# Kernel optimization log

Hardware: AMD Instinct MI355X
Metric: run time of the kernel (lower is better)

The kernel has to match this reference:

```python
import jax, jax.numpy as jnp
import numpy as np

MASK_THRED = 1        # init kwarg mask_thred
TRIPLE_WEIGHT = 1.0   # init kwarg triple_weight (scales gradient of shifted branch)
NEG = -1e30
EPS = 1e-8


def setup_inputs() -> dict:
    key = jax.random.key(0)
    k1, k2 = jax.random.split(key)
    x = jax.random.normal(k1, (2, 128, 96, 96), dtype=jnp.float32)
    mask = jax.random.randint(k2, (96, 96), 0, 2, dtype=jnp.int32)
    return {"x": x, "mask": mask}


def reference(x, mask):
    # x: (B, C, H, W); former = x[:, :C//2], latter = x[:, C//2:]
    B, C, H, W = x.shape
    c2 = C // 2
    hw = H * W

    # shift_sz=1, stride=1, mask_thred=1 -> a location is 'masked' iff mask >= 1
    flag = mask.reshape(hw) >= MASK_THRED  # (hw,) True = inside hole

    former, latter = x[:, :c2], x[:, c2:]

    # similarity path is non-differentiable in the original (hard argmax, detached latter)
    lat = jax.lax.stop_gradient(latter).reshape(B, c2, hw).transpose(0, 2, 1)  # (B, hw, c2)
    # original normalizes only the candidate (non-masked) patches (NCC filters)
    lat_n = lat / jnp.maximum(jnp.linalg.norm(lat, axis=-1, keepdims=True), EPS)

    # cross-correlation of every location against every (normalized) candidate
    sim = jnp.einsum('bic,bjc->bij', lat, lat_n)  # (B, hw, hw)
    # only non-masked locations are valid candidates j
    sim = jnp.where(flag[None, None, :], NEG, sim)
    idx = jnp.argmax(sim, axis=-1)  # (B, hw) nearest non-masked neighbor per location

    # shift: copy the FORMER feature from the matched non-masked location
    fmr = former.reshape(B, c2, hw).transpose(0, 2, 1)  # (B, hw, c2)
    gathered = jnp.take_along_axis(fmr, idx[:, :, None], axis=1)  # (B, hw, c2)

    # triple_weight scales only the gradient of the shifted branch (fwd unchanged)
    tw = jnp.float32(TRIPLE_WEIGHT)
    gathered = gathered * tw + jax.lax.stop_gradient(gathered * (1.0 - tw))

    # shifted features only at masked locations, zero elsewhere
    shift = jnp.where(flag[None, :, None], gathered, jnp.float32(0.0))
    shift = shift.transpose(0, 2, 1).reshape(B, c2, H, W)

    # triple: (former, latter, shifted) -> (B, 3*C//2, H, W)
    return jnp.concatenate([former, latter, shift], axis=1)
```

## Files before the change

### kernel.cpp

```cpp
#include <hip/hip_runtime.h>
#include <math.h>

#define HW 9216
#define C2 64
#define NSTRIP 288
#define NCH 16
#define EPSN 1e-8f

typedef _Float16 f16x8  __attribute__((ext_vector_type(8)));
typedef float    f32x16 __attribute__((ext_vector_type(16)));

__global__ void prep_kernel(const float* __restrict__ x, const int* __restrict__ mask,
                            int* __restrict__ ilist, int* __restrict__ jlist,
                            int* __restrict__ slotmap, int* __restrict__ counts,
                            float* __restrict__ invAll, unsigned long long* __restrict__ amax) {
    if (blockIdx.x < 576) {
        int t = blockIdx.x * 256 + threadIdx.x;
        int cc = t & 7;
        int pb = t >> 3;
        int b = pb / HW, p = pb - b * HW;
        const float* xl = x + (size_t)(b * 128 + 64) * HW + p;
        float ss = 0.f;
#pragma unroll
        for (int e = 0; e < 8; e++) { float w = xl[(size_t)(cc * 8 + e) * HW]; ss = fmaf(w, w, ss); }
        ss += __shfl_xor(ss, 1, 64);
        ss += __shfl_xor(ss, 2, 64);
        ss += __shfl_xor(ss, 4, 64);
        if (cc == 0) {
            invAll[pb] = 1.0f / fmaxf(sqrtf(ss), EPSN);
            amax[pb] = 0ull;
        }
    } else {
        int t = threadIdx.x;
        int base = t * 36;
        unsigned long long fl = 0ull; int cnt = 0;
#pragma unroll
        for (int k = 0; k < 36; k++) {
            int f = (mask[base + k] >= 1) ? 1 : 0;
            fl |= (unsigned long long)f << k;
            cnt += f;
        }
        int lane = t & 63, wave = t >> 6;
        int v = cnt;
#pragma unroll
        for (int off = 1; off < 64; off <<= 1) {
            int u = __shfl_up(v, off, 64);
            if (lane >= off) v += u;
        }
        __shared__ int wsum[4];
        if (lane == 63) wsum[wave] = v;
        __syncthreads();
        int woff = 0;
#pragma unroll
        for (int w = 0; w < 4; w++) if (w < wave) woff += wsum[w];
        int incl = v + woff;
        int excl = incl - cnt;
        int posF = excl, posU = base - excl;
#pragma unroll
        for (int k = 0; k < 36; k++) {
            int p = base + k;
            if ((fl >> k) & 1ull) { slotmap[p] = posF | 0x80000000; ilist[posF++] = p; }
            else                  { slotmap[p] = posU;              jlist[posU++] = p; }
        }
        if (t == 255) { counts[0] = incl; counts[1] = HW - incl; }
    }
}

__global__ void pack_kernel(const float* __restrict__ x, const int* __restrict__ slotmap,
                            const float* __restrict__ invAll,
                            _Float16* __restrict__ aH, _Float16* __restrict__ aL,
                            _Float16* __restrict__ bH, _Float16* __restrict__ bL) {
    int p = blockIdx.x * 256 + threadIdx.x;
    int cc = blockIdx.y;
    int b = blockIdx.z;
    int sm = slotmap[p];
    int flagged = (sm >> 31) & 1;
    int slot = sm & 0x7fffffff;
    const float* xl = x + (size_t)(b * 128 + 64) * HW + p;
    float scale = flagged ? 1.0f : invAll[b * HW + p];
    f16x8 hh, ll;
#pragma unroll
    for (int e = 0; e < 8; e++) {
        float w = xl[(size_t)(cc * 8 + e) * HW] * scale;
        _Float16 h = (_Float16)w;
        hh[e] = h;
        ll[e] = (_Float16)((w - (float)h) * 2048.0f);
    }
    int ks = cc >> 1, g = cc & 1;
    int strip = slot >> 5, ln = slot & 31;
    size_t off = ((((size_t)b * NSTRIP + strip) * 4 + ks) * 64 + (g * 32 + ln)) * 8;
    _Float16* dh = flagged ? aH : bH;
    _Float16* dl = flagged ? aL : bL;
    *(f16x8*)(dh + off) = hh;
    *(f16x8*)(dl + off) = ll;
}

__device__ __forceinline__ unsigned int ordf(float f) {
    unsigned int u = __float_as_uint(f);
    return (u & 0x80000000u) ? ~u : (u | 0x80000000u);
}

__global__ __launch_bounds__(256, 2) void argmax_kernel(
    const _Float16* __restrict__ aH, const _Float16* __restrict__ aL,
    const _Float16* __restrict__ bH, const _Float16* __restrict__ bL,
    const int* __restrict__ ilist, const int* __restrict__ counts,
    unsigned long long* __restrict__ amax)
{
    int ni = counts[0];
    if (blockIdx.x * 256 >= ni) return;
    int nj = counts[1];
    int njt = (nj + 31) >> 5;
    int tpc = (njt + NCH - 1) / NCH;
    int s = blockIdx.y;
    int jt0 = s * tpc, jt1 = min(jt0 + tpc, njt);
    if (jt0 >= jt1) return;
    int b = blockIdx.z;
    int wave = threadIdx.x >> 6, l = threadIdx.x & 63;
    int base = (blockIdx.x * 4 + wave) * 64;
    int g = l >> 5, ln = l & 31;
    int strip0 = base >> 5;

    __shared__ f16x8 lds[2][8][64];

    const f16x8* apH = (const f16x8*)aH + ((size_t)b * NSTRIP + strip0) * 256 + l;
    const f16x8* apL = (const f16x8*)aL + ((size_t)b * NSTRIP + strip0) * 256 + l;
    f16x8 xh0 = apH[0],   xh1 = apH[64],  xh2 = apH[128], xh3 = apH[192];
    f16x8 xl0 = apL[0],   xl1 = apL[64],  xl2 = apL[128], xl3 = apL[192];
    f16x8 yh0 = apH[256], yh1 = apH[320], yh2 = apH[384], yh3 = apH[448];
    f16x8 yl0 = apL[256], yl1 = apL[320], yl2 = apL[384], yl3 = apL[448];

    int f0 = wave * 2;
    const f16x8* s0 = (const f16x8*)((f0 < 4) ? bH : bL) +
                      (size_t)b * NSTRIP * 256 + (size_t)(f0 & 3) * 64 + l;
    const f16x8* s1 = (const f16x8*)((f0 + 1 < 4) ? bH : bL) +
                      (size_t)b * NSTRIP * 256 + (size_t)((f0 + 1) & 3) * 64 + l;

    {
        f16x8 t0 = s0[(size_t)jt0 * 256];
        f16x8 t1 = s1[(size_t)jt0 * 256];
        lds[0][f0][l] = t0;
        lds[0][f0 + 1][l] = t1;
    }
    __syncthreads();

    float bv0 = -INFINITY, bv1 = -INFINITY;
    int bj0 = -1, bj1 = -1;
    int cur = 0;

    for (int jt = jt0; jt < jt1; ++jt, cur ^= 1) {
        f16x8 n0, n1;
        bool more = (jt + 1 < jt1);
        if (more) {
            n0 = s0[(size_t)(jt + 1) * 256];
            n1 = s1[(size_t)(jt + 1) * 256];
        }
        f16x8 bh0 = lds[cur][0][l], bh1 = lds[cur][1][l];
        f16x8 bh2 = lds[cur][2][l], bh3 = lds[cur][3][l];
        f16x8 bl0 = lds[cur][4][l], bl1 = lds[cur][5][l];
        f16x8 bl2 = lds[cur][6][l], bl3 = lds[cur][7][l];
        f32x16 cH0 = {}, cC0 = {}, cH1 = {}, cC1 = {};
        cH0 = __builtin_amdgcn_mfma_f32_32x32x16_f16(bh0, xh0, cH0, 0, 0, 0);
        cC0 = __builtin_amdgcn_mfma_f32_32x32x16_f16(bh0, xl0, cC0, 0, 0, 0);
        cC0 = __builtin_amdgcn_mfma_f32_32x32x16_f16(bl0, xh0, cC0, 0, 0, 0);
        cH0 = __builtin_amdgcn_mfma_f32_32x32x16_f16(bh1, xh1, cH0, 0, 0, 0);
        cC0 = __builtin_amdgcn_mfma_f32_32x32x16_f16(bh1, xl1, cC0, 0, 0, 0);
        cC0 = __builtin_amdgcn_mfma_f32_32x32x16_f16(bl1, xh1, cC0, 0, 0, 0);
        cH0 = __builtin_amdgcn_mfma_f32_32x32x16_f16(bh2, xh2, cH0, 0, 0, 0);
        cC0 = __builtin_amdgcn_mfma_f32_32x32x16_f16(bh2, xl2, cC0, 0, 0, 0);
        cC0 = __builtin_amdgcn_mfma_f32_32x32x16_f16(bl2, xh2, cC0, 0, 0, 0);
        cH0 = __builtin_amdgcn_mfma_f32_32x32x16_f16(bh3, xh3, cH0, 0, 0, 0);
        cC0 = __builtin_amdgcn_mfma_f32_32x32x16_f16(bh3, xl3, cC0, 0, 0, 0);
        cC0 = __builtin_amdgcn_mfma_f32_32x32x16_f16(bl3, xh3, cC0, 0, 0, 0);
        cH1 = __builtin_amdgcn_mfma_f32_32x32x16_f16(bh0, yh0, cH1, 0, 0, 0);
        cC1 = __builtin_amdgcn_mfma_f32_32x32x16_f16(bh0, yl0, cC1, 0, 0, 0);
        cC1 = __builtin_amdgcn_mfma_f32_32x32x16_f16(bl0, yh0, cC1, 0, 0, 0);
        cH1 = __builtin_amdgcn_mfma_f32_32x32x16_f16(bh1, yh1, cH1, 0, 0, 0);
        cC1 = __builtin_amdgcn_mfma_f32_32x32x16_f16(bh1, yl1, cC1, 0, 0, 0);
        cC1 = __builtin_amdgcn_mfma_f32_32x32x16_f16(bl1, yh1, cC1, 0, 0, 0);
        cH1 = __builtin_amdgcn_mfma_f32_32x32x16_f16(bh2, yh2, cH1, 0, 0, 0);
        cC1 = __builtin_amdgcn_mfma_f32_32x32x16_f16(bh2, yl2, cC1, 0, 0, 0);
        cC1 = __builtin_amdgcn_mfma_f32_32x32x16_f16(bl2, yh2, cC1, 0, 0, 0);
        cH1 = __builtin_amdgcn_mfma_f32_32x32x16_f16(bh3, yh3, cH1, 0, 0, 0);
        cC1 = __builtin_amdgcn_mfma_f32_32x32x16_f16(bh3, yl3, cC1, 0, 0, 0);
        cC1 = __builtin_amdgcn_mfma_f32_32x32x16_f16(bl3, yh3, cC1, 0, 0, 0);
        int jb = jt << 5;
#pragma unroll
        for (int r = 0; r < 16; ++r) {
            int row = (r & 3) + 8 * (r >> 2) + 4 * g;
            int j = jb + row;
            float v0 = fmaf(cC0[r], 4.8828125e-4f , cH0[r]);
            float v1 = fmaf(cC1[r], 4.8828125e-4f, cH1[r]);
            if (j < nj && v0 > bv0) { bv0 = v0; bj0 = j; }
            if (j < nj && v1 > bv1) { bv1 = v1; bj1 = j; }
        }
        if (more) {
            lds[cur ^ 1][f0][l] = n0;
            lds[cur ^ 1][f0 + 1][l] = n1;
        }
        __syncthreads();
    }

    unsigned long long k0 = ((unsigned long long)ordf(bv0) << 32) |
                            (unsigned long long)(~(unsigned int)bj0);
    unsigned long long k1 = ((unsigned long long)ordf(bv1) << 32) |
                            (unsigned long long)(~(unsigned int)bj1);
    unsigned long long o0 = __shfl_xor(k0, 32, 64);
    unsigned long long o1 = __shfl_xor(k1, 32, 64);
    if (o0 > k0) k0 = o0;
    if (o1 > k1) k1 = o1;
    int il0 = base + ln, il1 = base + 32 + ln;
    if (g == 0) {
        if (il0 < ni && (unsigned)(k0 >> 32) > 0x007FFFFFu)
            atomicMax(&amax[(size_t)b * HW + ilist[il0]], k0);
        if (il1 < ni && (unsigned)(k1 >> 32) > 0x007FFFFFu)
            atomicMax(&amax[(size_t)b * HW + ilist[il1]], k1);
    }
}

__global__ void epilogue_kernel(const float4* __restrict__ x4, const float* __restrict__ x,
                                const int* __restrict__ mask,
                                const unsigned long long* __restrict__ amax,
                                const int* __restrict__ jlist, float4* __restrict__ out4) {
    const int q = HW / 4;
    int t = blockIdx.x * blockDim.x + threadIdx.x;
    if (t >= 2 * 192 * q) return;
    int pos4 = t % q;
    int c = (t / q) % 192;
    int b = t / (192 * q);
    if (c < 128) {
        out4[t] = x4[((size_t)b * 128 + c) * q + pos4];
    } else {
        float4 v = make_float4(0.f, 0.f, 0.f, 0.f);
        float* vp = &v.x;
        int pos = pos4 * 4;
        const float* xf = x + (size_t)(b * 128 + (c - 128)) * HW;
#pragma unroll
        for (int k = 0; k < 4; k++) {
            int p = pos + k;
            if (mask[p] >= 1) {
                unsigned long long key = amax[(size_t)b * HW + p];
                int j = 0;
                if (key != 0ull) j = jlist[(int)(~(unsigned int)key)];
                vp[k] = xf[j];
            }
        }
        out4[t] = v;
    }
}

extern "C" void kernel_launch(void* const* d_in, const int* in_sizes, int n_in,
                              void* d_out, int out_size, void* d_ws, size_t ws_size,
                              hipStream_t stream) {
    const float* x = (const float*)d_in[0];
    const int* mask = (const int*)d_in[1];
    float4* out4 = (float4*)d_out;

    char* ws = (char*)d_ws;
    int*   counts  = (int*)ws;
    int*   ilist   = (int*)(ws + 128);
    int*   jlist   = (int*)(ws + 36992);
    int*   slotmap = (int*)(ws + 73856);
    unsigned long long* amax = (unsigned long long*)(ws + 110720);
    float* invAll  = (float*)(ws + 258176);
    _Float16* aH = (_Float16*)(ws + 331904);
    _Float16* aL = (_Float16*)(ws + 331904 + 1 * 2359296);
    _Float16* bH = (_Float16*)(ws + 331904 + 2 * 2359296);
    _Float16* bL = (_Float16*)(ws + 331904 + 3 * 2359296);

    prep_kernel<<<577, 256, 0, stream>>>(x, mask, ilist, jlist, slotmap, counts,
                                         invAll, amax);
    {
        dim3 grid(HW / 256, 8, 2);
        pack_kernel<<<grid, 256, 0, stream>>>(x, slotmap, invAll, aH, aL, bH, bL);
    }
    {
        dim3 grid(NSTRIP / 8, NCH, 2);
        argmax_kernel<<<grid, 256, 0, stream>>>(aH, aL, bH, bL, ilist, counts, amax);
    }
    {
        int n = 2 * 192 * (HW / 4);
        epilogue_kernel<<<(n + 255) / 256, 256, 0, stream>>>((const float4*)x, x, mask,
                                                             amax, jlist, out4);
    }
}
```

Measured before the change: 109.7 us.

## Drop mask compaction; compute full dense similarity with bitmask filtering

```diff
diff --git a/kernel.cpp b/kernel.cpp
--- a/kernel.cpp
+++ b/kernel.cpp
@@ -2,7 +2,6 @@
 #include <math.h>
 
 #define HW 9216
-#define C2 64
 #define NSTRIP 288
 #define NCH 16
 #define EPSN 1e-8f
@@ -11,88 +10,52 @@
 typedef float    f32x16 __attribute__((ext_vector_type(16)));
 
 __global__ void prep_kernel(const float* __restrict__ x, const int* __restrict__ mask,
-                            int* __restrict__ ilist, int* __restrict__ jlist,
-                            int* __restrict__ slotmap, int* __restrict__ counts,
-                            float* __restrict__ invAll, unsigned long long* __restrict__ amax) {
-    if (blockIdx.x < 576) {
-        int t = blockIdx.x * 256 + threadIdx.x;
-        int cc = t & 7;
-        int pb = t >> 3;
-        int b = pb / HW, p = pb - b * HW;
-        const float* xl = x + (size_t)(b * 128 + 64) * HW + p;
-        float ss = 0.f;
-#pragma unroll
-        for (int e = 0; e < 8; e++) { float w = xl[(size_t)(cc * 8 + e) * HW]; ss = fmaf(w, w, ss); }
-        ss += __shfl_xor(ss, 1, 64);
-        ss += __shfl_xor(ss, 2, 64);
-        ss += __shfl_xor(ss, 4, 64);
-        if (cc == 0) {
-            invAll[pb] = 1.0f / fmaxf(sqrtf(ss), EPSN);
-            amax[pb] = 0ull;
-        }
-    } else {
-        int t = threadIdx.x;
-        int base = t * 36;
-        unsigned long long fl = 0ull; int cnt = 0;
-#pragma unroll
-        for (int k = 0; k < 36; k++) {
-            int f = (mask[base + k] >= 1) ? 1 : 0;
-            fl |= (unsigned long long)f << k;
-            cnt += f;
-        }
-        int lane = t & 63, wave = t >> 6;
-        int v = cnt;
-#pragma unroll
-        for (int off = 1; off < 64; off <<= 1) {
-            int u = __shfl_up(v, off, 64);
-            if (lane >= off) v += u;
-        }
-        __shared__ int wsum[4];
-        if (lane == 63) wsum[wave] = v;
-        __syncthreads();
-        int woff = 0;
-#pragma unroll
-        for (int w = 0; w < 4; w++) if (w < wave) woff += wsum[w];
-        int incl = v + woff;
-        int excl = incl - cnt;
-        int posF = excl, posU = base - excl;
-#pragma unroll
-        for (int k = 0; k < 36; k++) {
-            int p = base + k;
-            if ((fl >> k) & 1ull) { slotmap[p] = posF | 0x80000000; ilist[posF++] = p; }
-            else                  { slotmap[p] = posU;              jlist[posU++] = p; }
-        }
-        if (t == 255) { counts[0] = incl; counts[1] = HW - incl; }
-    }
-}
-
-__global__ void pack_kernel(const float* __restrict__ x, const int* __restrict__ slotmap,
-                            const float* __restrict__ invAll,
+                            unsigned* __restrict__ fw, unsigned long long* __restrict__ amax,
                             _Float16* __restrict__ aH, _Float16* __restrict__ aL,
                             _Float16* __restrict__ bH, _Float16* __restrict__ bL) {
-    int p = blockIdx.x * 256 + threadIdx.x;
-    int cc = blockIdx.y;
-    int b = blockIdx.z;
-    int sm = slotmap[p];
-    int flagged = (sm >> 31) & 1;
-    int slot = sm & 0x7fffffff;
+    if (blockIdx.x == 288) {
+        for (int w = threadIdx.x; w < NSTRIP; w += 256) {
+            const int* mp = mask + w * 32;
+            unsigned m = 0;
+#pragma unroll
+            for (int k = 0; k < 32; k++) m |= (mp[k] >= 1 ? 1u : 0u) << k;
+            fw[w] = m;
+        }
+        return;
+    }
+    int t = blockIdx.x * 256 + threadIdx.x;
+    int sub = t & 63;
+    int q = sub >> 4;
+    int pb = ((t >> 6) << 4) | (sub & 15);
+    int b = pb / HW, p = pb - b * HW;
     const float* xl = x + (size_t)(b * 128 + 64) * HW + p;
-    float scale = flagged ? 1.0f : invAll[b * HW + p];
-    f16x8 hh, ll;
-#pragma unroll
-    for (int e = 0; e < 8; e++) {
-        float w = xl[(size_t)(cc * 8 + e) * HW] * scale;
-        _Float16 h = (_Float16)w;
-        hh[e] = h;
-        ll[e] = (_Float16)((w - (float)h) * 2048.0f);
-    }
-    int ks = cc >> 1, g = cc & 1;
-    int strip = slot >> 5, ln = slot & 31;
-    size_t off = ((((size_t)b * NSTRIP + strip) * 4 + ks) * 64 + (g * 32 + ln)) * 8;
-    _Float16* dh = flagged ? aH : bH;
-    _Float16* dl = flagged ? aL : bL;
-    *(f16x8*)(dh + off) = hh;
-    *(f16x8*)(dl + off) = ll;
+    float v[16]; float ss = 0.f;
+#pragma unroll
+    for (int e = 0; e < 16; e++) { float w0 = xl[(size_t)(q * 16 + e) * HW]; v[e] = w0; ss = fmaf(w0, w0, ss); }
+    ss += __shfl_xor(ss, 16, 64);
+    ss += __shfl_xor(ss, 32, 64);
+    float inv = 1.0f / fmaxf(sqrtf(ss), EPSN);
+    if (q == 0) amax[pb] = 0ull;
+    int tile = p >> 5, lnp = p & 31;
+#pragma unroll
+    for (int h = 0; h < 2; h++) {
+        size_t off = ((((size_t)b * NSTRIP + tile) * 4 + q) * 64 + h * 32 + lnp) * 8;
+        f16x8 hh, ll;
+#pragma unroll
+        for (int e = 0; e < 8; e++) {
+            float w0 = v[h * 8 + e];
+            _Float16 hv = (_Float16)w0;
+            hh[e] = hv; ll[e] = (_Float16)((w0 - (float)hv) * 2048.0f);
+        }
+        *(f16x8*)(aH + off) = hh; *(f16x8*)(aL + off) = ll;
+#pragma unroll
+        for (int e = 0; e < 8; e++) {
+            float w0 = v[h * 8 + e] * inv;
+            _Float16 hv = (_Float16)w0;
+            hh[e] = hv; ll[e] = (_Float16)((w0 - (float)hv) * 2048.0f);
+        }
+        *(f16x8*)(bH + off) = hh; *(f16x8*)(bL + off) = ll;
+    }
 }
 
 __device__ __forceinline__ unsigned int ordf(float f) {
@@ -103,18 +66,11 @@
 __global__ __launch_bounds__(256, 2) void argmax_kernel(
     const _Float16* __restrict__ aH, const _Float16* __restrict__ aL,
     const _Float16* __restrict__ bH, const _Float16* __restrict__ bL,
-    const int* __restrict__ ilist, const int* __restrict__ counts,
-    unsigned long long* __restrict__ amax)
+    const unsigned* __restrict__ fw, unsigned long long* __restrict__ amax)
 {
-    int ni = counts[0];
-    if (blockIdx.x * 256 >= ni) return;
-    int nj = counts[1];
-    int njt = (nj + 31) >> 5;
-    int tpc = (njt + NCH - 1) / NCH;
-    int s = blockIdx.y;
-    int jt0 = s * tpc, jt1 = min(jt0 + tpc, njt);
-    if (jt0 >= jt1) return;
-    int b = blockIdx.z;
+    const int tpc = NSTRIP / NCH;
+    int b = blockIdx.z, s = blockIdx.y;
+    int jt0 = s * tpc, jt1 = jt0 + tpc;
     int wave = threadIdx.x >> 6, l = threadIdx.x & 63;
     int base = (blockIdx.x * 4 + wave) * 64;
     int g = l >> 5, ln = l & 31;
@@ -184,14 +140,18 @@
         cC1 = __builtin_amdgcn_mfma_f32_32x32x16_f16(bh3, yl3, cC1, 0, 0, 0);
         cC1 = __builtin_amdgcn_mfma_f32_32x32x16_f16(bl3, yh3, cC1, 0, 0, 0);
         int jb = jt << 5;
+        unsigned fmg = fw[jt] >> (4 * g);
 #pragma unroll
         for (int r = 0; r < 16; ++r) {
-            int row = (r & 3) + 8 * (r >> 2) + 4 * g;
-            int j = jb + row;
+            int rowc = (r & 3) + 8 * (r >> 2);
+            bool ok = ((fmg >> rowc) & 1u) == 0u;
+            int j = jb + rowc + 4 * g;
             float v0 = fmaf(cC0[r], 4.8828125e-4f , cH0[r]);
             float v1 = fmaf(cC1[r], 4.8828125e-4f, cH1[r]);
-            if (j < nj && v0 > bv0) { bv0 = v0; bj0 = j; }
-            if (j < nj && v1 > bv1) { bv1 = v1; bj1 = j; }
+            v0 = ok ? v0 : -INFINITY;
+            v1 = ok ? v1 : -INFINITY;
+            if (v0 > bv0) { bv0 = v0; bj0 = j; }
+            if (v1 > bv1) { bv1 = v1; bj1 = j; }
         }
         if (more) {
             lds[cur ^ 1][f0][l] = n0;
@@ -210,17 +170,17 @@
     if (o1 > k1) k1 = o1;
     int il0 = base + ln, il1 = base + 32 + ln;
     if (g == 0) {
-        if (il0 < ni && (unsigned)(k0 >> 32) > 0x007FFFFFu)
-            atomicMax(&amax[(size_t)b * HW + ilist[il0]], k0);
-        if (il1 < ni && (unsigned)(k1 >> 32) > 0x007FFFFFu)
-            atomicMax(&amax[(size_t)b * HW + ilist[il1]], k1);
+        if (((fw[il0 >> 5] >> (il0 & 31)) & 1u) && (unsigned)(k0 >> 32) > 0x007FFFFFu)
+            atomicMax(&amax[(size_t)b * HW + il0], k0);
+        if (((fw[il1 >> 5] >> (il1 & 31)) & 1u) && (unsigned)(k1 >> 32) > 0x007FFFFFu)
+            atomicMax(&amax[(size_t)b * HW + il1], k1);
     }
 }
 
 __global__ void epilogue_kernel(const float4* __restrict__ x4, const float* __restrict__ x,
                                 const int* __restrict__ mask,
                                 const unsigned long long* __restrict__ amax,
-                                const int* __restrict__ jlist, float4* __restrict__ out4) {
+                                float4* __restrict__ out4) {
     const int q = HW / 4;
     int t = blockIdx.x * blockDim.x + threadIdx.x;
     if (t >= 2 * 192 * q) return;
@@ -240,7 +200,7 @@
             if (mask[p] >= 1) {
                 unsigned long long key = amax[(size_t)b * HW + p];
                 int j = 0;
-                if (key != 0ull) j = jlist[(int)(~(unsigned int)key)];
+                if (key != 0ull) j = (int)(~(unsigned int)key);
                 vp[k] = xf[j];
             }
         }
@@ -256,30 +216,21 @@
     float4* out4 = (float4*)d_out;
 
     char* ws = (char*)d_ws;
-    int*   counts  = (int*)ws;
-    int*   ilist   = (int*)(ws + 128);
-    int*   jlist   = (int*)(ws + 36992);
-    int*   slotmap = (int*)(ws + 73856);
-    unsigned long long* amax = (unsigned long long*)(ws + 110720);
-    float* invAll  = (float*)(ws + 258176);
-    _Float16* aH = (_Float16*)(ws + 331904);
-    _Float16* aL = (_Float16*)(ws + 331904 + 1 * 2359296);
-    _Float16* bH = (_Float16*)(ws + 331904 + 2 * 2359296);
-    _Float16* bL = (_Float16*)(ws + 331904 + 3 * 2359296);
-
-    prep_kernel<<<577, 256, 0, stream>>>(x, mask, ilist, jlist, slotmap, counts,
-                                         invAll, amax);
-    {
-        dim3 grid(HW / 256, 8, 2);
-        pack_kernel<<<grid, 256, 0, stream>>>(x, slotmap, invAll, aH, aL, bH, bL);
-    }
+    unsigned* fw = (unsigned*)(ws + 128);
+    unsigned long long* amax = (unsigned long long*)(ws + 4096);
+    _Float16* aH = (_Float16*)(ws + 151552);
+    _Float16* aL = (_Float16*)(ws + 151552 + 1 * 2359296);
+    _Float16* bH = (_Float16*)(ws + 151552 + 2 * 2359296);
+    _Float16* bL = (_Float16*)(ws + 151552 + 3 * 2359296);
+
+    prep_kernel<<<289, 256, 0, stream>>>(x, mask, fw, amax, aH, aL, bH, bL);
     {
         dim3 grid(NSTRIP / 8, NCH, 2);
-        argmax_kernel<<<grid, 256, 0, stream>>>(aH, aL, bH, bL, ilist, counts, amax);
+        argmax_kernel<<<grid, 256, 0, stream>>>(aH, aL, bH, bL, fw, amax);
     }
     {
         int n = 2 * 192 * (HW / 4);
         epilogue_kernel<<<(n + 255) / 256, 256, 0, stream>>>((const float4*)x, x, mask,
-                                                             amax, jlist, out4);
-    }
-}
+                                                             amax, out4);
+    }
+}
```

New measurement: 144.1 us. 1.31x slower.

## Fuse mask scan, norm computation and fp16 packing into one prep kernel

Applied to the files above, without the earlier changes.

```diff
diff --git a/kernel.cpp b/kernel.cpp
--- a/kernel.cpp
+++ b/kernel.cpp
@@ -2,7 +2,6 @@
 #include <math.h>
 
 #define HW 9216
-#define C2 64
 #define NSTRIP 288
 #define NCH 16
 #define EPSN 1e-8f
@@ -10,89 +9,83 @@
 typedef _Float16 f16x8  __attribute__((ext_vector_type(8)));
 typedef float    f32x16 __attribute__((ext_vector_type(16)));
 
-__global__ void prep_kernel(const float* __restrict__ x, const int* __restrict__ mask,
-                            int* __restrict__ ilist, int* __restrict__ jlist,
-                            int* __restrict__ slotmap, int* __restrict__ counts,
-                            float* __restrict__ invAll, unsigned long long* __restrict__ amax) {
-    if (blockIdx.x < 576) {
-        int t = blockIdx.x * 256 + threadIdx.x;
-        int cc = t & 7;
-        int pb = t >> 3;
-        int b = pb / HW, p = pb - b * HW;
-        const float* xl = x + (size_t)(b * 128 + 64) * HW + p;
-        float ss = 0.f;
-#pragma unroll
-        for (int e = 0; e < 8; e++) { float w = xl[(size_t)(cc * 8 + e) * HW]; ss = fmaf(w, w, ss); }
-        ss += __shfl_xor(ss, 1, 64);
-        ss += __shfl_xor(ss, 2, 64);
-        ss += __shfl_xor(ss, 4, 64);
-        if (cc == 0) {
-            invAll[pb] = 1.0f / fmaxf(sqrtf(ss), EPSN);
-            amax[pb] = 0ull;
-        }
-    } else {
-        int t = threadIdx.x;
-        int base = t * 36;
-        unsigned long long fl = 0ull; int cnt = 0;
-#pragma unroll
-        for (int k = 0; k < 36; k++) {
-            int f = (mask[base + k] >= 1) ? 1 : 0;
-            fl |= (unsigned long long)f << k;
-            cnt += f;
-        }
-        int lane = t & 63, wave = t >> 6;
-        int v = cnt;
-#pragma unroll
-        for (int off = 1; off < 64; off <<= 1) {
-            int u = __shfl_up(v, off, 64);
-            if (lane >= off) v += u;
-        }
-        __shared__ int wsum[4];
-        if (lane == 63) wsum[wave] = v;
-        __syncthreads();
-        int woff = 0;
-#pragma unroll
-        for (int w = 0; w < 4; w++) if (w < wave) woff += wsum[w];
-        int incl = v + woff;
-        int excl = incl - cnt;
-        int posF = excl, posU = base - excl;
-#pragma unroll
-        for (int k = 0; k < 36; k++) {
-            int p = base + k;
-            if ((fl >> k) & 1ull) { slotmap[p] = posF | 0x80000000; ilist[posF++] = p; }
-            else                  { slotmap[p] = posU;              jlist[posU++] = p; }
-        }
-        if (t == 255) { counts[0] = incl; counts[1] = HW - incl; }
-    }
-}
-
-__global__ void pack_kernel(const float* __restrict__ x, const int* __restrict__ slotmap,
-                            const float* __restrict__ invAll,
-                            _Float16* __restrict__ aH, _Float16* __restrict__ aL,
-                            _Float16* __restrict__ bH, _Float16* __restrict__ bL) {
-    int p = blockIdx.x * 256 + threadIdx.x;
-    int cc = blockIdx.y;
-    int b = blockIdx.z;
-    int sm = slotmap[p];
-    int flagged = (sm >> 31) & 1;
-    int slot = sm & 0x7fffffff;
+__global__ __launch_bounds__(256) void prep_kernel(
+    const float* __restrict__ x, const int* __restrict__ mask,
+    int* __restrict__ ilist, int* __restrict__ jlist, int* __restrict__ counts,
+    _Float16* __restrict__ aH, _Float16* __restrict__ aL,
+    _Float16* __restrict__ bH, _Float16* __restrict__ bL,
+    unsigned long long* __restrict__ amax)
+{
+    __shared__ unsigned short slot16[HW];
+    __shared__ int wsum[4];
+    int tid = threadIdx.x;
+    int base = tid * 36;
+    const int4* mp4 = (const int4*)mask + tid * 9;
+    unsigned long long fl = 0ull; int cnt = 0;
+#pragma unroll
+    for (int k4 = 0; k4 < 9; k4++) {
+        int4 m4 = mp4[k4];
+        int f0 = (m4.x >= 1), f1 = (m4.y >= 1), f2 = (m4.z >= 1), f3 = (m4.w >= 1);
+        fl |= ((unsigned long long)f0 << (k4 * 4)) | ((unsigned long long)f1 << (k4 * 4 + 1)) |
+              ((unsigned long long)f2 << (k4 * 4 + 2)) | ((unsigned long long)f3 << (k4 * 4 + 3));
+        cnt += f0 + f1 + f2 + f3;
+    }
+    int lane = tid & 63, wave = tid >> 6;
+    int v = cnt;
+#pragma unroll
+    for (int off = 1; off < 64; off <<= 1) {
+        int u = __shfl_up(v, off, 64);
+        if (lane >= off) v += u;
+    }
+    if (lane == 63) wsum[wave] = v;
+    __syncthreads();
+    int woff = 0;
+#pragma unroll
+    for (int w = 0; w < 4; w++) if (w < wave) woff += wsum[w];
+    int incl = v + woff;
+    int excl = incl - cnt;
+    int posF = excl, posU = base - excl;
+    bool wl = (blockIdx.x == 0);
+#pragma unroll
+    for (int k = 0; k < 36; k++) {
+        int p = base + k;
+        if ((fl >> k) & 1ull) { slot16[p] = (unsigned short)(posF | 0x8000); if (wl) ilist[posF] = p; posF++; }
+        else                  { slot16[p] = (unsigned short)posU;            if (wl) jlist[posU] = p; posU++; }
+    }
+    if (wl && tid == 255) { counts[0] = incl; counts[1] = HW - incl; }
+    __syncthreads();
+    int t = blockIdx.x * 256 + tid;
+    int sub = t & 63;
+    int q = sub >> 4;
+    int pb = ((t >> 6) << 4) | (sub & 15);
+    int b = pb / HW, p = pb - b * HW;
     const float* xl = x + (size_t)(b * 128 + 64) * HW + p;
-    float scale = flagged ? 1.0f : invAll[b * HW + p];
-    f16x8 hh, ll;
-#pragma unroll
-    for (int e = 0; e < 8; e++) {
-        float w = xl[(size_t)(cc * 8 + e) * HW] * scale;
-        _Float16 h = (_Float16)w;
-        hh[e] = h;
-        ll[e] = (_Float16)((w - (float)h) * 2048.0f);
-    }
-    int ks = cc >> 1, g = cc & 1;
-    int strip = slot >> 5, ln = slot & 31;
-    size_t off = ((((size_t)b * NSTRIP + strip) * 4 + ks) * 64 + (g * 32 + ln)) * 8;
+    float vv[16]; float ss = 0.f;
+#pragma unroll
+    for (int e = 0; e < 16; e++) { float w0 = xl[(size_t)(q * 16 + e) * HW]; vv[e] = w0; ss = fmaf(w0, w0, ss); }
+    ss += __shfl_xor(ss, 16, 64);
+    ss += __shfl_xor(ss, 32, 64);
+    float inv = 1.0f / fmaxf(sqrtf(ss), EPSN);
+    if (q == 0) amax[pb] = 0ull;
+    unsigned sl = slot16[p];
+    int flagged = sl >> 15;
+    int slot = sl & 0x7fff;
+    float scale = flagged ? 1.0f : inv;
+    int tile = slot >> 5, lnp = slot & 31;
     _Float16* dh = flagged ? aH : bH;
     _Float16* dl = flagged ? aL : bL;
-    *(f16x8*)(dh + off) = hh;
-    *(f16x8*)(dl + off) = ll;
+#pragma unroll
+    for (int h = 0; h < 2; h++) {
+        size_t off = ((((size_t)b * NSTRIP + tile) * 4 + q) * 64 + h * 32 + lnp) * 8;
+        f16x8 hh, ll;
+#pragma unroll
+        for (int e = 0; e < 8; e++) {
+            float w0 = vv[h * 8 + e] * scale;
+            _Float16 hv = (_Float16)w0;
+            hh[e] = hv; ll[e] = (_Float16)((w0 - (float)hv) * 2048.0f);
+        }
+        *(f16x8*)(dh + off) = hh; *(f16x8*)(dl + off) = ll;
+    }
 }
 
 __device__ __forceinline__ unsigned int ordf(float f) {
@@ -256,23 +249,17 @@
     float4* out4 = (float4*)d_out;
 
     char* ws = (char*)d_ws;
-    int*   counts  = (int*)ws;
-    int*   ilist   = (int*)(ws + 128);
-    int*   jlist   = (int*)(ws + 36992);
-    int*   slotmap = (int*)(ws + 73856);
-    unsigned long long* amax = (unsigned long long*)(ws + 110720);
-    float* invAll  = (float*)(ws + 258176);
-    _Float16* aH = (_Float16*)(ws + 331904);
-    _Float16* aL = (_Float16*)(ws + 331904 + 1 * 2359296);
-    _Float16* bH = (_Float16*)(ws + 331904 + 2 * 2359296);
-    _Float16* bL = (_Float16*)(ws + 331904 + 3 * 2359296);
-
-    prep_kernel<<<577, 256, 0, stream>>>(x, mask, ilist, jlist, slotmap, counts,
-                                         invAll, amax);
-    {
-        dim3 grid(HW / 256, 8, 2);
-        pack_kernel<<<grid, 256, 0, stream>>>(x, slotmap, invAll, aH, aL, bH, bL);
-    }
+    int*   counts = (int*)ws;
+    int*   ilist  = (int*)(ws + 128);
+    int*   jlist  = (int*)(ws + 36992);
+    unsigned long long* amax = (unsigned long long*)(ws + 73856);
+    _Float16* aH = (_Float16*)(ws + 221312);
+    _Float16* aL = (_Float16*)(ws + 221312 + 1 * 2359296);
+    _Float16* bH = (_Float16*)(ws + 221312 + 2 * 2359296);
+    _Float16* bL = (_Float16*)(ws + 221312 + 3 * 2359296);
+
+    prep_kernel<<<288, 256, 0, stream>>>(x, mask, ilist, jlist, counts,
+                                         aH, aL, bH, bL, amax);
     {
         dim3 grid(NSTRIP / 8, NCH, 2);
         argmax_kernel<<<grid, 256, 0, stream>>>(aH, aL, bH, bL, ilist, counts, amax);
```

Result: faster. 101.8 us (-7.1%).
